# Optimization experiments

Measured on AMD Instinct MI355X. Metric: run time of the kernel, lower is better.

Reference implementation:

```python
import jax, jax.numpy as jnp
import numpy as np

T, B, D, H = 256, 256, 512, 1024


def setup_inputs() -> dict:
    key = jax.random.key(0)
    ks = jax.random.split(key, 9)
    s = 0.02  # small init scale for numerical sanity
    return {
        "inputs": jax.random.normal(ks[0], (T, B, D), dtype=jnp.float32),
        "Wf": jax.random.normal(ks[1], (D + H, H), dtype=jnp.float32) * s,
        "bf": jax.random.normal(ks[2], (H,), dtype=jnp.float32) * s,
        "Wi": jax.random.normal(ks[3], (D + H, H), dtype=jnp.float32) * s,
        "bi": jax.random.normal(ks[4], (H,), dtype=jnp.float32) * s,
        "Wg": jax.random.normal(ks[5], (D + H, H), dtype=jnp.float32) * s,
        "bg": jax.random.normal(ks[6], (H,), dtype=jnp.float32) * s,
        "Wo": jax.random.normal(ks[7], (D + H, H), dtype=jnp.float32) * s,
        "bo": jax.random.normal(ks[8], (H,), dtype=jnp.float32) * s,
    }


def reference(inputs, Wf, bf, Wi, bi, Wg, bg, Wo, bo):
    hidden_dim = Wf.shape[1]
    batch = inputs.shape[1]
    # Fuse the four gate projections into one [D+H, 4H] GEMM per step.
    W = jnp.concatenate([Wf, Wi, Wg, Wo], axis=1)   # [D+H, 4H]
    b = jnp.concatenate([bf, bi, bg, bo], axis=0)   # [4H]

    h0 = jnp.zeros((batch, hidden_dim), dtype=inputs.dtype)
    c0 = jnp.zeros((batch, hidden_dim), dtype=inputs.dtype)

    def step(carry, x):
        hx, cx = carry
        combined = jnp.concatenate([x, hx], axis=1)  # [B, D+H]
        z = combined @ W + b                          # [B, 4H]
        f, i, g, o = jnp.split(z, 4, axis=1)
        f = jax.nn.sigmoid(f)
        i = jax.nn.sigmoid(i)
        g = jnp.tanh(g)
        o = jax.nn.sigmoid(o)
        cx = f * cx + i * g
        hx = o * jnp.tanh(cx)
        return (hx, cx), hx

    (hx, cx), outputs = jax.lax.scan(step, (h0, c0), inputs)
    return outputs, hx, cx
```

## Files before the change

kernel.cpp:

```cpp
#include <hip/hip_runtime.h>
#include <cstdint>
#include <cstddef>

#define T_STEPS 256
#define BATCH   256
#define DIN     512
#define HID     1024
#define KTOT    1536
#define NOUT    4096
#define BHSZ    ((size_t)BATCH * HID)

typedef __bf16 bf16;
typedef __bf16 bf16x4 __attribute__((ext_vector_type(4)));
typedef __bf16 bf16x8 __attribute__((ext_vector_type(8)));
typedef float  f32x4  __attribute__((ext_vector_type(4)));

__device__ __forceinline__ void store_bf16_sc(bf16* p, bf16 v) {
  unsigned short u = __builtin_bit_cast(unsigned short, v);
  asm volatile("global_store_short %0, %1, off sc0 sc1" :: "v"(p), "v"(u) : "memory");
}

#define VMW_(N) asm volatile("s_waitcnt vmcnt(" #N ")" ::: "memory")
#define VMW(N) do { VMW_(N); __builtin_amdgcn_sched_barrier(0); } while (0)
#define LGKM0() do { asm volatile("s_waitcnt lgkmcnt(0)" ::: "memory"); \
                     __builtin_amdgcn_sched_barrier(0); } while (0)
#define SBAR() __builtin_amdgcn_sched_barrier(0)
#define RAWBAR() do { SBAR(); __builtin_amdgcn_s_barrier(); SBAR(); } while (0)

__device__ __forceinline__ float fexp2(float x) {
  float r; asm("v_exp_f32 %0, %1" : "=v"(r) : "v"(x)); return r;
}
__device__ __forceinline__ float frcp(float x) {
  float r; asm("v_rcp_f32 %0, %1" : "=v"(r) : "v"(x)); return r;
}
__device__ __forceinline__ float fsigmoid(float x) {
  return frcp(1.f + fexp2(-1.44269504f * x));
}
__device__ __forceinline__ float ftanh(float x) {
  return 1.f - 2.f * frcp(1.f + fexp2(2.88539008f * x));
}

__global__ void convert_w_kernel(const float* __restrict__ Wf, const float* __restrict__ Wi,
                                 const float* __restrict__ Wg, const float* __restrict__ Wo,
                                 bf16* __restrict__ Wt) {
  __shared__ float tile[64][17];
  const int k0 = blockIdx.x * 64;
  const int jb = blockIdx.y;
  const int j0 = jb * 16;
  const int t  = threadIdx.x;
  const float* srcs[4] = {Wf, Wi, Wg, Wo};
#pragma unroll
  for (int g = 0; g < 4; ++g) {
    const float* src = srcs[g];
    {
      const int jl = t & 15, kb = t >> 4;
#pragma unroll
      for (int r = 0; r < 4; ++r) {
        const int kl = kb + 16 * r;
        tile[kl][jl] = src[(size_t)(k0 + kl) * HID + (j0 + jl)];
      }
    }
    __syncthreads();
    {
      const int kk = t & 63, jl4 = t >> 6;
#pragma unroll
      for (int r = 0; r < 4; ++r) {
        const int jl = jl4 + 4 * r;
        Wt[(size_t)(jb * 64 + g * 16 + jl) * KTOT + (k0 + kk)] = (bf16)tile[kk][jl];
      }
    }
    __syncthreads();
  }
}

__global__ void convert_x_kernel(const float* __restrict__ X, bf16* __restrict__ xb) {
  const int t = blockIdx.y;
  const int i = blockIdx.x * blockDim.x + threadIdx.x;
  const float4 v = ((const float4*)(X + (size_t)t * BATCH * DIN))[i];
  bf16x4 o;
  o[0] = (bf16)v.x; o[1] = (bf16)v.y; o[2] = (bf16)v.z; o[3] = (bf16)v.w;
  ((bf16x4*)(xb + (size_t)t * BATCH * DIN))[i] = o;
}

__global__ __launch_bounds__(512, 2)
void lstm_v13(const bf16* __restrict__ Bt,
              const bf16* __restrict__ xb,
              bf16* __restrict__ hseq,
              const bf16* __restrict__ zb16,
              float* __restrict__ outF,
              const float* __restrict__ bf_, const float* __restrict__ bi_,
              const float* __restrict__ bg_, const float* __restrict__ bo_,
              unsigned* __restrict__ flags) {
  __shared__ f32x4 redu[8][8][64];

  const int tid = threadIdx.x, lane = tid & 63, wid = tid >> 6;
  const int bid = blockIdx.x;
  const int e8  = bid & 7;
  const int mh   = e8 >> 1;
  const int nblk = ((bid >> 3) << 1) | (e8 & 1);
  const int bn0 = nblk * 64;
  const int fr = lane & 15, fq = lane >> 4;
  const int rowA = mh * 32, rowB = 128 + mh * 32;

  if (tid == 0)
    (void)__hip_atomic_load(flags, __ATOMIC_ACQUIRE, __HIP_MEMORY_SCOPE_AGENT);
  __syncthreads();

  const int j = nblk * 16 + fr;
  const float bfv = bf_[j], biv = bi_[j], bgv = bg_[j], bov = bo_[j];
  float crA = 0.f, crB = 0.f;

  bf16x8 breg[6][4];
#pragma unroll
  for (int s = 0; s < 6; ++s) {
    const int ks = wid + 8 * s;
#pragma unroll
    for (int nf = 0; nf < 4; ++nf)
      breg[s][nf] = *(const bf16x8*)(Bt + (size_t)(bn0 + nf * 16 + fr) * KTOT
                                     + ks * 32 + fq * 8);
  }

  bf16x8 xA0[2], xA1[2], xB0[2], xB1[2], h2[2], h3[2], h4[2], h5[2];

  auto ldx = [&](int t2, int rowbase, int s, bf16x8 (&sl)[2]) {
    const bf16* src = xb + (size_t)t2 * BATCH * DIN + (wid + 8 * s) * 32 + fq * 8;
#pragma unroll
    for (int mf = 0; mf < 2; ++mf)
      sl[mf] = *(const bf16x8*)(src + (size_t)(rowbase + mf * 16 + fr) * DIN);
  };
  auto ldh = [&](int t2, int half, int s, bf16x8 (&sl)[2]) {
    const int c0 = (wid + 8 * s) * 32 - 512;
    const int pp = (c0 >> 4) + (fq >> 1);
    const bf16* base = (t2 == 0)
        ? zb16
        : hseq + ((((size_t)(t2 - 1) * 2 + half) << 8) + mh * 64 + pp) * 512;
    const int coloff = (fq & 1) * 8;
#pragma unroll
    for (int mf = 0; mf < 2; ++mf)
      sl[mf] = *(const bf16x8*)(base + (mf * 16 + fr) * 16 + coloff);
  };

  const int pn8 = 2 * wid + ((lane & 7) >> 1) * 16 + (lane & 1);
  auto pollh = [&](int tprev, int half) {
    const unsigned* f = flags + (((size_t)tprev * 2 + half) << 8) + mh * 64 + pn8;
    const unsigned long long tt0 = __builtin_amdgcn_s_memrealtime();
    for (;;) {
      unsigned v = __hip_atomic_load(f, __ATOMIC_RELAXED,
                                     __HIP_MEMORY_SCOPE_AGENT);
      if (__all(v != 0)) break;
      __builtin_amdgcn_s_sleep(1);
      if (__builtin_amdgcn_s_memrealtime() - tt0 > (1ULL << 22)) break;
    }
    asm volatile("" ::: "memory");
    __builtin_amdgcn_sched_barrier(0);
  };

  auto dump = [&](f32x4 (&acc)[2][4]) {
#pragma unroll
    for (int mf = 0; mf < 2; ++mf)
#pragma unroll
      for (int nf = 0; nf < 4; ++nf)
        redu[wid][mf * 4 + nf][lane] = acc[mf][nf];
  };

  auto finish = [&](int t2, int half, float& cre) {
    const int mf_c = wid >> 2;
    const int lsel = (wid & 3) * 16 + fr;
    float z[4];
#pragma unroll
    for (int nf = 0; nf < 4; ++nf) {
      float s_ = 0.f;
#pragma unroll
      for (int s = 0; s < 8; ++s)
        s_ += ((const float*)&redu[s][mf_c * 4 + nf][lsel])[fq];
      z[nf] = s_;
    }
    const float fg = fsigmoid(z[0] + bfv);
    const float ig = fsigmoid(z[1] + biv);
    const float gg = ftanh(z[2] + bgv);
    const float og = fsigmoid(z[3] + bov);
    cre = fg * cre + ig * gg;
    const float h = og * ftanh(cre);
    bf16* tile = hseq + ((((size_t)t2 * 2 + half) << 8) + mh * 64 + nblk) * 512;
    store_bf16_sc(&tile[wid * 64 + lane], (bf16)h);
    const int rowg = half * 128 + mh * 32 + wid * 4 + fq;
    outF[(size_t)t2 * BHSZ + (size_t)rowg * HID + j] = h;
    if (t2 == T_STEPS - 1)
      outF[(size_t)(T_STEPS + 1) * BHSZ + (size_t)rowg * HID + j] = cre;
  };

  auto setflag = [&](int t2, int half) {
    __hip_atomic_store(&flags[(((size_t)t2 * 2 + half) << 8) + mh * 64 + nblk],
                       1u, __ATOMIC_RELAXED, __HIP_MEMORY_SCOPE_AGENT);
  };

#define MFMA8(ACC, SL, S) do {                                              \
    __builtin_amdgcn_s_setprio(1);                                          \
    _Pragma("unroll")                                                       \
    for (int mf_ = 0; mf_ < 2; ++mf_) {                                     \
      _Pragma("unroll")                                                     \
      for (int nf_ = 0; nf_ < 4; ++nf_)                                     \
        ACC[mf_][nf_] = __builtin_amdgcn_mfma_f32_16x16x32_bf16(            \
            SL[mf_], breg[S][nf_], ACC[mf_][nf_], 0, 0, 0);                 \
    }                                                                       \
    __builtin_amdgcn_s_setprio(0);                                          \
  } while (0)

  ldx(0, rowA, 0, xA0); SBAR(); ldx(0, rowA, 1, xA1); SBAR();
  ldx(0, rowB, 0, xB0); SBAR(); ldx(0, rowB, 1, xB1); SBAR();
  VMW(4);

#pragma unroll 1
  for (int t = 0; t < T_STEPS; ++t) {
    f32x4 accA[2][4] = {}, accB[2][4] = {};
    MFMA8(accA, xA0, 0); MFMA8(accA, xA1, 1);
    if (t > 0) pollh(t - 1, 0);
    ldh(t, 0, 2, h2); SBAR(); ldh(t, 0, 3, h3); SBAR();
    ldh(t, 0, 4, h4); SBAR(); ldh(t, 0, 5, h5); SBAR();
    VMW(8);
    MFMA8(accB, xB0, 0); MFMA8(accB, xB1, 1);
    VMW(6); MFMA8(accA, h2, 2);
    VMW(4); MFMA8(accA, h3, 3);
    VMW(2); MFMA8(accA, h4, 4);
    VMW(0); MFMA8(accA, h5, 5);
    dump(accA); LGKM0(); RAWBAR();
    if (t > 0) pollh(t - 1, 1);
    ldh(t, 1, 2, h2); SBAR(); ldh(t, 1, 3, h3); SBAR();
    ldh(t, 1, 4, h4); SBAR(); ldh(t, 1, 5, h5); SBAR();
    finish(t, 0, crA);
    if (t + 1 < T_STEPS) {
      ldx(t + 1, rowA, 0, xA0); SBAR(); ldx(t + 1, rowA, 1, xA1); SBAR();
      VMW(5);
    } else {
      VMW(0);
    }
    RAWBAR();
    if (tid == 0) setflag(t, 0);
    MFMA8(accB, h2, 2); MFMA8(accB, h3, 3);
    MFMA8(accB, h4, 4); MFMA8(accB, h5, 5);
    dump(accB); LGKM0(); RAWBAR();
    finish(t, 1, crB);
    if (t + 1 < T_STEPS) {
      ldx(t + 1, rowB, 0, xB0); SBAR(); ldx(t + 1, rowB, 1, xB1); SBAR();
      VMW(4);
    } else {
      VMW(0);
    }
    RAWBAR();
    if (tid == 0) setflag(t, 1);
  }
#undef MFMA8
}

__global__ __launch_bounds__(512, 2)
void lstm_fb(const bf16* __restrict__ Bt,
             const float* __restrict__ X,
             const float* __restrict__ zbF,
             float* __restrict__ outF,
             const float* __restrict__ bf_, const float* __restrict__ bi_,
             const float* __restrict__ bg_, const float* __restrict__ bo_,
             unsigned* __restrict__ flags) {
  __shared__ f32x4 redu[8][16][64];
  const int tid = threadIdx.x, lane = tid & 63, wid = tid >> 6;
  const int bid = blockIdx.x;
  const int xcd = bid & 7, sl = bid >> 3;
  const int nblk = xcd * 8 + (sl & 7);
  const int mblk = sl >> 3;
  const int bm0 = mblk * 64;
  const int bn0 = nblk * 64;
  const int fr = lane & 15, fq = lane >> 4;

  if (tid == 0)
    (void)__hip_atomic_load(flags, __ATOMIC_ACQUIRE, __HIP_MEMORY_SCOPE_AGENT);
  __syncthreads();

  const int j = nblk * 16 + fr;
  const float bfv = bf_[j], biv = bi_[j], bgv = bg_[j], bov = bo_[j];
  float cr[2] = {0.f, 0.f};

  bf16x8 breg[6][4];
#pragma unroll
  for (int s = 0; s < 6; ++s) {
    const int ks = wid + 8 * s;
#pragma unroll
    for (int nf = 0; nf < 4; ++nf)
      breg[s][nf] = *(const bf16x8*)(Bt + (size_t)(bn0 + nf * 16 + fr) * KTOT
                                     + ks * 32 + fq * 8);
  }

  bf16x8 afp[2][4];

  auto poll = [&](int tprev) {
    const unsigned* f = flags + (size_t)tprev * 256 + mblk * 64;
    const unsigned long long tt0 = __builtin_amdgcn_s_memrealtime();
    for (;;) {
      unsigned v = __hip_atomic_load(f + lane, __ATOMIC_RELAXED,
                                     __HIP_MEMORY_SCOPE_AGENT);
      if (__all(v != 0)) break;
      __builtin_amdgcn_s_sleep(2);
      if (__builtin_amdgcn_s_memrealtime() - tt0 > (1ULL << 22)) break;
    }
    asm volatile("" ::: "memory");
    __builtin_amdgcn_sched_barrier(0);
  };

  auto loadA = [&](int t2, int s, int p) __attribute__((always_inline)) {
    const int ks = wid + 8 * s;
    const int k = ks * 32 + fq * 8;
    if (s == 2 && t2 > 0) poll(t2 - 1);
    const float* src; int ld, kk;
    if (s < 2) { src = X + (size_t)t2 * BATCH * DIN; ld = DIN; kk = k; }
    else {
      src = (t2 == 0) ? zbF : outF + (size_t)(t2 - 1) * BHSZ;
      ld = HID; kk = k - 512;
    }
#pragma unroll
    for (int mf = 0; mf < 4; ++mf) {
      const float* q = src + (size_t)(bm0 + mf * 16 + fr) * ld + kk;
      const f32x4 lo = *(const f32x4*)q;
      const f32x4 hi = *(const f32x4*)(q + 4);
      bf16x8 v;
      v[0] = (bf16)lo[0]; v[1] = (bf16)lo[1]; v[2] = (bf16)lo[2]; v[3] = (bf16)lo[3];
      v[4] = (bf16)hi[0]; v[5] = (bf16)hi[1]; v[6] = (bf16)hi[2]; v[7] = (bf16)hi[3];
      afp[p][mf] = v;
    }
  };

  loadA(0, 0, 0);

#pragma unroll 1
  for (int t = 0; t < T_STEPS; ++t) {
    f32x4 acc[4][4] = {};
#pragma unroll
    for (int s = 0; s < 6; ++s) {
      if (s < 5)                loadA(t, s + 1, (s + 1) & 1);
      else if (t + 1 < T_STEPS) loadA(t + 1, 0, 0);
      __builtin_amdgcn_s_setprio(1);
#pragma unroll
      for (int mf = 0; mf < 4; ++mf)
#pragma unroll
        for (int nf = 0; nf < 4; ++nf)
          acc[mf][nf] = __builtin_amdgcn_mfma_f32_16x16x32_bf16(
              afp[s & 1][mf], breg[s][nf], acc[mf][nf], 0, 0, 0);
      __builtin_amdgcn_s_setprio(0);
    }

#pragma unroll
    for (int mf = 0; mf < 4; ++mf)
#pragma unroll
      for (int nf = 0; nf < 4; ++nf)
        redu[wid][mf * 4 + nf][lane] = acc[mf][nf];
    __syncthreads();

    const int fbase = (wid >> 1) * 4;
    const int rh = wid & 1;
    float z[2][4];
#pragma unroll
    for (int e = 0; e < 2; ++e) {
      const int rloc = rh * 8 + fq * 2 + e;
      const int lsel = (rloc >> 2) * 16 + fr;
      const int rc = rloc & 3;
#pragma unroll
      for (int nf = 0; nf < 4; ++nf) {
        float sum = 0.f;
#pragma unroll
        for (int s = 0; s < 8; ++s)
          sum += ((const float*)&redu[s][fbase + nf][lsel])[rc];
        z[e][nf] = sum;
      }
    }

    float* outSl = outF + (size_t)t * BHSZ;
#pragma unroll
    for (int e = 0; e < 2; ++e) {
      const float fg = 1.f / (1.f + expf(-(z[e][0] + bfv)));
      const float ig = 1.f / (1.f + expf(-(z[e][1] + biv)));
      const float gg = tanhf(z[e][2] + bgv);
      const float og = 1.f / (1.f + expf(-(z[e][3] + bov)));
      cr[e] = fg * cr[e] + ig * gg;
      const float h = og * tanhf(cr[e]);
      const int m = bm0 + wid * 8 + fq * 2 + e;
      const size_t off = (size_t)m * HID + j;
      __hip_atomic_store(&outSl[off], h, __ATOMIC_RELAXED,
                         __HIP_MEMORY_SCOPE_AGENT);
      if (t == T_STEPS - 1)
        outF[(size_t)(T_STEPS + 1) * BHSZ + off] = cr[e];
    }
    asm volatile("s_waitcnt vmcnt(0)" ::: "memory");
    __syncthreads();
    if (tid == 0)
      __hip_atomic_store(&flags[(size_t)t * 256 + mblk * 64 + nblk], 1u,
                         __ATOMIC_RELAXED, __HIP_MEMORY_SCOPE_AGENT);
  }
}

extern "C" void kernel_launch(void* const* d_in, const int* in_sizes, int n_in,
                              void* d_out, int out_size, void* d_ws, size_t ws_size,
                              hipStream_t stream) {
  const float* X   = (const float*)d_in[0];
  const float* Wf  = (const float*)d_in[1];
  const float* bf_ = (const float*)d_in[2];
  const float* Wi  = (const float*)d_in[3];
  const float* bi_ = (const float*)d_in[4];
  const float* Wg  = (const float*)d_in[5];
  const float* bg_ = (const float*)d_in[6];
  const float* Wo  = (const float*)d_in[7];
  const float* bo_ = (const float*)d_in[8];
  float* out = (float*)d_out;

  const size_t WtB   = (size_t)NOUT * KTOT * 2;
  const size_t zBb   = BHSZ * 4;
  const size_t flagB = (size_t)T_STEPS * 2 * 256 * 4;
  const size_t XbB   = (size_t)T_STEPS * BATCH * DIN * 2;
  const size_t HsB   = (size_t)T_STEPS * 2 * 256 * 1024;

  char* ws = (char*)d_ws;
  bf16*     Wt    = (bf16*)ws;              ws += WtB;
  float*    zbF   = (float*)(void*)ws;      ws += zBb;
  unsigned* flags = (unsigned*)(void*)ws;   ws += flagB;

  const bool big = ws_size >= WtB + zBb + flagB + XbB + HsB + (1u << 20);
  bf16* xbp = nullptr;  bf16* hseq = nullptr;
  if (big) {
    xbp  = (bf16*)ws;   ws += XbB;
    hseq = (bf16*)ws;
  }

  hipMemsetAsync(zbF, 0, zBb + flagB, stream);

  convert_w_kernel<<<dim3(KTOT / 64, NOUT / 64), 256, 0, stream>>>(Wf, Wi, Wg, Wo, Wt);

  if (big) {
    convert_x_kernel<<<dim3(BATCH * DIN / 4 / 256, T_STEPS), 256, 0, stream>>>(X, xbp);
    lstm_v13<<<256, 512, 0, stream>>>(Wt, xbp, hseq, (const bf16*)zbF, out,
                                      bf_, bi_, bg_, bo_, flags);
  } else {
    lstm_fb<<<256, 512, 0, stream>>>(Wt, X, zbF, out,
                                     bf_, bi_, bg_, bo_, flags);
  }

  hipMemcpyAsync(out + (size_t)T_STEPS * BHSZ, out + (size_t)(T_STEPS - 1) * BHSZ,
                 BHSZ * 4, hipMemcpyDeviceToDevice, stream);
}
```

Measured before the change: 1.903 ms.

## Rotate register buffers across two-step unrolled LSTM loop to prefetch both h halves early

Unrolls the recurrent time loop by two and rotates eight register slices between x and h roles. Both halves of the previous hidden state are now polled and loaded up front, and next-step x loads go into the freed registers. The aim is more memory-level parallelism and less exposed latency on the serial per-step critical path. The vmcnt accounting becomes more intricate, and the flag stores are delayed until after the next x prefetch issues, which may lengthen the cross-block dependency chain.

```diff
diff --git a/kernel.cpp b/kernel.cpp
--- a/kernel.cpp
+++ b/kernel.cpp
@@ -83,7 +83,7 @@
 }
 
 __global__ __launch_bounds__(512, 2)
-void lstm_v13(const bf16* __restrict__ Bt,
+void lstm_v14(const bf16* __restrict__ Bt,
               const bf16* __restrict__ xb,
               bf16* __restrict__ hseq,
               const bf16* __restrict__ zb16,
@@ -120,7 +120,7 @@
                                      + ks * 32 + fq * 8);
   }
 
-  bf16x8 xA0[2], xA1[2], xB0[2], xB1[2], h2[2], h3[2], h4[2], h5[2];
+  bf16x8 P0[2], P1[2], P2[2], P3[2], Q2[2], Q3[2], Q4[2], Q5[2];
 
   auto ldx = [&](int t2, int rowbase, int s, bf16x8 (&sl)[2]) {
     const bf16* src = xb + (size_t)t2 * BATCH * DIN + (wid + 8 * s) * 32 + fq * 8;
@@ -206,49 +206,61 @@
     __builtin_amdgcn_s_setprio(0);                                          \
   } while (0)
 
-  ldx(0, rowA, 0, xA0); SBAR(); ldx(0, rowA, 1, xA1); SBAR();
-  ldx(0, rowB, 0, xB0); SBAR(); ldx(0, rowB, 1, xB1); SBAR();
+#define STEP(T0, X0, X1, X2, X3, H2, H3, H4, H5) do {                       \
+    const int t_ = (T0);                                                    \
+    f32x4 accA[2][4] = {}, accB[2][4] = {};                                 \
+    VMW(4);                                                                 \
+    MFMA8(accA, X0, 0); MFMA8(accA, X1, 1);                                 \
+    if (t_ > 0) pollh(t_ - 1, 0);                                           \
+    ldh(t_, 0, 2, H2); ldh(t_, 0, 3, H3);                                   \
+    ldh(t_, 0, 4, H4); ldh(t_, 0, 5, H5); SBAR();                           \
+    VMW(8);                                                                 \
+    MFMA8(accB, X2, 0); MFMA8(accB, X3, 1);                                 \
+    if (t_ > 0) pollh(t_ - 1, 1);                                           \
+    ldh(t_, 1, 2, X0); ldh(t_, 1, 3, X1);                                   \
+    ldh(t_, 1, 4, X2); ldh(t_, 1, 5, X3); SBAR();                           \
+    VMW(14); MFMA8(accA, H2, 2);                                            \
+    VMW(12); MFMA8(accA, H3, 3);                                            \
+    VMW(10); MFMA8(accA, H4, 4);                                            \
+    VMW(8);  MFMA8(accA, H5, 5);                                            \
+    dump(accA); LGKM0(); RAWBAR();                                          \
+    finish(t_, 0, crA);                                                     \
+    if (t_ + 1 < T_STEPS) {                                                 \
+      ldx(t_ + 1, rowA, 0, H2); ldx(t_ + 1, rowA, 1, H3); SBAR();           \
+      VMW(6);                            \
+    } else {                                                                \
+      VMW(3);                                 \
+    }                                                                       \
+    RAWBAR();                   \
+    MFMA8(accB, X0, 2); MFMA8(accB, X1, 3);                                 \
+    MFMA8(accB, X2, 4); MFMA8(accB, X3, 5);                                 \
+    dump(accB); LGKM0(); RAWBAR();                                          \
+    finish(t_, 1, crB);                                                     \
+    if (t_ + 1 < T_STEPS) {                                                 \
+      ldx(t_ + 1, rowB, 0, H4); ldx(t_ + 1, rowB, 1, H5); SBAR();           \
+      VMW(6);                 \
+      if (tid == 0) setflag(t_, 0);                                         \
+      VMW(4);                                                 \
+      if (tid == 0) setflag(t_, 1);                                         \
+    } else {                                                                \
+      VMW(3);                                \
+      if (tid == 0) setflag(t_, 0);                                         \
+      VMW(0);                                                               \
+      if (tid == 0) setflag(t_, 1);                                         \
+    }                                                                       \
+    RAWBAR();                     \
+  } while (0)
+
+  ldx(0, rowA, 0, P0); SBAR(); ldx(0, rowA, 1, P1); SBAR();
+  ldx(0, rowB, 0, P2); SBAR(); ldx(0, rowB, 1, P3); SBAR();
   VMW(4);
 
 #pragma unroll 1
-  for (int t = 0; t < T_STEPS; ++t) {
-    f32x4 accA[2][4] = {}, accB[2][4] = {};
-    MFMA8(accA, xA0, 0); MFMA8(accA, xA1, 1);
-    if (t > 0) pollh(t - 1, 0);
-    ldh(t, 0, 2, h2); SBAR(); ldh(t, 0, 3, h3); SBAR();
-    ldh(t, 0, 4, h4); SBAR(); ldh(t, 0, 5, h5); SBAR();
-    VMW(8);
-    MFMA8(accB, xB0, 0); MFMA8(accB, xB1, 1);
-    VMW(6); MFMA8(accA, h2, 2);
-    VMW(4); MFMA8(accA, h3, 3);
-    VMW(2); MFMA8(accA, h4, 4);
-    VMW(0); MFMA8(accA, h5, 5);
-    dump(accA); LGKM0(); RAWBAR();
-    if (t > 0) pollh(t - 1, 1);
-    ldh(t, 1, 2, h2); SBAR(); ldh(t, 1, 3, h3); SBAR();
-    ldh(t, 1, 4, h4); SBAR(); ldh(t, 1, 5, h5); SBAR();
-    finish(t, 0, crA);
-    if (t + 1 < T_STEPS) {
-      ldx(t + 1, rowA, 0, xA0); SBAR(); ldx(t + 1, rowA, 1, xA1); SBAR();
-      VMW(5);
-    } else {
-      VMW(0);
-    }
-    RAWBAR();
-    if (tid == 0) setflag(t, 0);
-    MFMA8(accB, h2, 2); MFMA8(accB, h3, 3);
-    MFMA8(accB, h4, 4); MFMA8(accB, h5, 5);
-    dump(accB); LGKM0(); RAWBAR();
-    finish(t, 1, crB);
-    if (t + 1 < T_STEPS) {
-      ldx(t + 1, rowB, 0, xB0); SBAR(); ldx(t + 1, rowB, 1, xB1); SBAR();
-      VMW(4);
-    } else {
-      VMW(0);
-    }
-    RAWBAR();
-    if (tid == 0) setflag(t, 1);
-  }
+  for (int t = 0; t < T_STEPS; t += 2) {
+    STEP(t,     P0, P1, P2, P3, Q2, Q3, Q4, Q5);
+    STEP(t + 1, Q2, Q3, Q4, Q5, P0, P1, P2, P3);
+  }
+#undef STEP
 #undef MFMA8
 }
 
@@ -432,7 +444,7 @@
 
   if (big) {
     convert_x_kernel<<<dim3(BATCH * DIN / 4 / 256, T_STEPS), 256, 0, stream>>>(X, xbp);
-    lstm_v13<<<256, 512, 0, stream>>>(Wt, xbp, hseq, (const bf16*)zbF, out,
+    lstm_v14<<<256, 512, 0, stream>>>(Wt, xbp, hseq, (const bf16*)zbF, out,
                                       bf_, bi_, bg_, bo_, flags);
   } else {
     lstm_fb<<<256, 512, 0, stream>>>(Wt, X, zbF, out,
```

Result: slower. 2.162 ms (+13.6%).
